# Kernel optimization log

Hardware: AMD Instinct MI355X
Metric: run time of the kernel (lower is better)

Reference implementation:

```python
import jax, jax.numpy as jnp
import numpy as np

NP_, B_ = 44, 400000

def setup_inputs() -> dict:
    key = jax.random.key(0)
    k_x, k1, k2, k3, k4 = jax.random.split(key, 5)
    return {
        "X": jax.random.normal(k_x, (NP_, 1, B_), dtype=jnp.float32),
        "lin1s": jax.random.normal(k1, (NP_, 4, 1), dtype=jnp.float32),
        "lin2s": jax.random.normal(k2, (NP_, 8, 4), dtype=jnp.float32),
        "lin3s": jax.random.normal(k3, (NP_, 4, 8), dtype=jnp.float32),
        "lin4s": jax.random.normal(k4, (NP_, 1, 4), dtype=jnp.float32),
    }

def reference(X, lin1s, lin2s, lin3s, lin4s):
    # forward_all: chained batched tiny GEMMs with ReLU, 'lik,lkj->lij'
    h = jax.nn.relu(jnp.einsum('lik,lkj->lij', lin1s, X))   # (NP, 4, B)
    h = jax.nn.relu(jnp.einsum('lik,lkj->lij', lin2s, h))   # (NP, 8, B)
    h = jax.nn.relu(jnp.einsum('lik,lkj->lij', lin3s, h))   # (NP, 4, B)
    return jnp.einsum('lik,lkj->lij', lin4s, h)             # (NP, 1, B)
```

## Files before the change

kernel.cpp:

```cpp
#include <hip/hip_runtime.h>

#define NP    44
#define B     400000
#define B4    (B / 4)
#define BLK   256
#define GX    46
#define STRIDE (GX * BLK)
#define FULL_ITERS 8

typedef float v4f __attribute__((ext_vector_type(4)));

__global__ __launch_bounds__(64) void collapse_kernel(
    const float* __restrict__ W1, const float* __restrict__ W2,
    const float* __restrict__ W3, const float* __restrict__ W4,
    float2* __restrict__ g)
{
    const int l = threadIdx.x;
    if (l >= NP) return;
    const float* p1 = W1 + l * 4;
    const float* p2 = W2 + l * 32;
    const float* p3 = W3 + l * 32;
    const float* p4 = W4 + l * 4;

    float w1p[4], w1n[4];
#pragma unroll
    for (int k = 0; k < 4; ++k) {
        float w = p1[k];
        w1p[k] = fmaxf(w, 0.0f);
        w1n[k] = fminf(w, 0.0f);
    }
    float d2p[8], d2n[8];
#pragma unroll
    for (int i = 0; i < 8; ++i) {
        float ap = 0.0f, an = 0.0f;
#pragma unroll
        for (int k = 0; k < 4; ++k) {
            float w = p2[i * 4 + k];
            ap = fmaf(w, w1p[k], ap);
            an = fmaf(w, w1n[k], an);
        }
        d2p[i] = fmaxf(ap, 0.0f);
        d2n[i] = fminf(an, 0.0f);
    }
    float f3p[4], f3n[4];
#pragma unroll
    for (int j = 0; j < 4; ++j) {
        float ap = 0.0f, an = 0.0f;
#pragma unroll
        for (int i = 0; i < 8; ++i) {
            float w = p3[j * 8 + i];
            ap = fmaf(w, d2p[i], ap);
            an = fmaf(w, d2n[i], an);
        }
        f3p[j] = fmaxf(ap, 0.0f);
        f3n[j] = fminf(an, 0.0f);
    }
    float gp = 0.0f, gn = 0.0f;
#pragma unroll
    for (int j = 0; j < 4; ++j) {
        gp = fmaf(p4[j], f3p[j], gp);
        gn = fmaf(p4[j], f3n[j], gn);
    }
    g[l] = make_float2(gp, gn);
}

__device__ __forceinline__ v4f scale4(v4f v, float gp, float gn) {
    v4f r;
    r.x = v.x * (v.x >= 0.0f ? gp : gn);
    r.y = v.y * (v.y >= 0.0f ? gp : gn);
    r.z = v.z * (v.z >= 0.0f ? gp : gn);
    r.w = v.w * (v.w >= 0.0f ? gp : gn);
    return r;
}

__global__ __launch_bounds__(BLK) void stream_kernel(
    const float* __restrict__ X,
    const float2* __restrict__ g,
    float* __restrict__ out)
{
    const int l = blockIdx.y;
    const float2 gg = g[l];
    const float gp = gg.x, gn = gg.y;

    const v4f* Xp = (const v4f*)(X + (size_t)l * B);
    v4f*       Op = (v4f*)(out + (size_t)l * B);

    const int base = blockIdx.x * BLK + threadIdx.x;

#pragma unroll
    for (int it = 0; it < FULL_ITERS; ++it) {
        const int idx = base + it * STRIDE;
        v4f v = Xp[idx];
        Op[idx] = scale4(v, gp, gn);
    }
    {
        const int idx = base + FULL_ITERS * STRIDE;
        if (idx < B4) {
            v4f v = Xp[idx];
            Op[idx] = scale4(v, gp, gn);
        }
    }
}

extern "C" void kernel_launch(void* const* d_in, const int* in_sizes, int n_in,
                              void* d_out, int out_size, void* d_ws, size_t ws_size,
                              hipStream_t stream) {
    const float* X  = (const float*)d_in[0];
    const float* W1 = (const float*)d_in[1];
    const float* W2 = (const float*)d_in[2];
    const float* W3 = (const float*)d_in[3];
    const float* W4 = (const float*)d_in[4];
    float* out = (float*)d_out;
    float2* g = (float2*)d_ws;

    collapse_kernel<<<dim3(1), 64, 0, stream>>>(W1, W2, W3, W4, g);
    stream_kernel<<<dim3(GX, NP), BLK, 0, stream>>>(X, g, out);
}
```

Before: 128.2 us.

## Fuse weight collapse into streaming kernel with nontemporal loads and prefetch

Drops the separate single-block collapse kernel and has each thread compute the per-layer scalar gains inline from the weights, overlapping that work with the first X load. This removes one kernel launch and the dependency through workspace memory. It also switches loads and stores to nontemporal and software-pipelines the loop so the next load is issued before the current store. The cost is that every thread redundantly recomputes the small weight collapse.

```diff
diff --git a/kernel.cpp b/kernel.cpp
--- a/kernel.cpp
+++ b/kernel.cpp
@@ -10,18 +10,11 @@
 
 typedef float v4f __attribute__((ext_vector_type(4)));
 
-__global__ __launch_bounds__(64) void collapse_kernel(
-    const float* __restrict__ W1, const float* __restrict__ W2,
-    const float* __restrict__ W3, const float* __restrict__ W4,
-    float2* __restrict__ g)
+__device__ __forceinline__ void collapse_weights(
+    const float* __restrict__ p1, const float* __restrict__ p2,
+    const float* __restrict__ p3, const float* __restrict__ p4,
+    float& gp, float& gn)
 {
-    const int l = threadIdx.x;
-    if (l >= NP) return;
-    const float* p1 = W1 + l * 4;
-    const float* p2 = W2 + l * 32;
-    const float* p3 = W3 + l * 32;
-    const float* p4 = W4 + l * 4;
-
     float w1p[4], w1n[4];
 #pragma unroll
     for (int k = 0; k < 4; ++k) {
@@ -55,13 +48,12 @@
         f3p[j] = fmaxf(ap, 0.0f);
         f3n[j] = fminf(an, 0.0f);
     }
-    float gp = 0.0f, gn = 0.0f;
+    gp = 0.0f; gn = 0.0f;
 #pragma unroll
     for (int j = 0; j < 4; ++j) {
         gp = fmaf(p4[j], f3p[j], gp);
         gn = fmaf(p4[j], f3n[j], gn);
     }
-    g[l] = make_float2(gp, gn);
 }
 
 __device__ __forceinline__ v4f scale4(v4f v, float gp, float gn) {
@@ -73,31 +65,37 @@
     return r;
 }
 
-__global__ __launch_bounds__(BLK) void stream_kernel(
+__global__ __launch_bounds__(BLK) void collapsed_mlp_kernel(
     const float* __restrict__ X,
-    const float2* __restrict__ g,
+    const float* __restrict__ W1, const float* __restrict__ W2,
+    const float* __restrict__ W3, const float* __restrict__ W4,
     float* __restrict__ out)
 {
-    const int l = blockIdx.y;
-    const float2 gg = g[l];
-    const float gp = gg.x, gn = gg.y;
+    const int l    = blockIdx.y;
+    const int base = blockIdx.x * BLK + threadIdx.x;
 
     const v4f* Xp = (const v4f*)(X + (size_t)l * B);
     v4f*       Op = (v4f*)(out + (size_t)l * B);
 
-    const int base = blockIdx.x * BLK + threadIdx.x;
+    v4f v = __builtin_nontemporal_load(&Xp[base]);
+
+    float gp, gn;
+    collapse_weights(W1 + l * 4, W2 + l * 32, W3 + l * 32, W4 + l * 4, gp, gn);
 
 #pragma unroll
-    for (int it = 0; it < FULL_ITERS; ++it) {
-        const int idx = base + it * STRIDE;
-        v4f v = Xp[idx];
-        Op[idx] = scale4(v, gp, gn);
+    for (int it = 0; it < FULL_ITERS - 1; ++it) {
+        v4f vn = __builtin_nontemporal_load(&Xp[base + (it + 1) * STRIDE]);
+        __builtin_nontemporal_store(scale4(v, gp, gn), &Op[base + it * STRIDE]);
+        v = vn;
     }
+    __builtin_nontemporal_store(scale4(v, gp, gn),
+                                &Op[base + (FULL_ITERS - 1) * STRIDE]);
+
     {
         const int idx = base + FULL_ITERS * STRIDE;
         if (idx < B4) {
-            v4f v = Xp[idx];
-            Op[idx] = scale4(v, gp, gn);
+            v4f t = __builtin_nontemporal_load(&Xp[idx]);
+            __builtin_nontemporal_store(scale4(t, gp, gn), &Op[idx]);
         }
     }
 }
@@ -111,8 +109,6 @@
     const float* W3 = (const float*)d_in[3];
     const float* W4 = (const float*)d_in[4];
     float* out = (float*)d_out;
-    float2* g = (float2*)d_ws;
 
-    collapse_kernel<<<dim3(1), 64, 0, stream>>>(W1, W2, W3, W4, g);
-    stream_kernel<<<dim3(GX, NP), BLK, 0, stream>>>(X, g, out);
+    collapsed_mlp_kernel<<<dim3(GX, NP), BLK, 0, stream>>>(X, W1, W2, W3, W4, out);
 }
```

After: 130.3 us. About the same (+1.6%).
